# Kernel optimization log

Measured on AMD Instinct MI355X. Metric: run time of the kernel, lower is better.

The kernel has to match this reference:

```python
import jax, jax.numpy as jnp
import numpy as np
import math

TOPK = 32

def setup_inputs() -> dict:
    key = jax.random.key(0)
    k1, k2, k3, k4 = jax.random.split(key, 4)
    B, D_e, D_o, T, H, W = 2, 128, 256, 16, 64, 64
    H_ref = W_ref = 32  # resolution_ref = 2
    THW_ref = T * H_ref * W_ref
    HW_ref = H_ref * W_ref
    return {
        "m_in": jax.random.normal(k1, (B, D_e, T, H, W), jnp.float32),
        "m_out": jax.random.normal(k2, (B, D_o, T, H, W), jnp.float32),
        "q_in": jax.random.normal(k3, (B, D_e, H, W), jnp.float32),
        "qk_ref": jax.random.normal(k4, (B, THW_ref, HW_ref), jnp.float32),
    }


def reference(m_in, m_out, q_in, qk_ref):
    B, D_e, T, H, W = m_in.shape
    D_o = m_out.shape[1]
    _, THW_ref, HW_ref = qk_ref.shape
    res = int(math.sqrt(H * W // HW_ref))
    H_ref, W_ref = H // res, W // res
    s = res
    k = TOPK

    # top-k memory blocks for each of the HW_ref query blocks
    topk_val, topk_idx = jax.lax.top_k(jnp.swapaxes(qk_ref, 1, 2), k)  # [B, HW_ref, k]
    # torch path scatters one-hot then uses nonzero -> gather order is ascending-index;
    # softmax-attention over n is permutation invariant, but sort for exact faithfulness.
    idx_sorted = jnp.sort(topk_idx, axis=-1)

    def blockify(m, D):
        # [B,D,T,H,W] -> [B, T*H_ref*W_ref, s, s, D]
        m = m.reshape(B, D, T, H_ref, s, W_ref, s)
        m = m.transpose(0, 2, 3, 5, 4, 6, 1)  # B,T,H_ref,W_ref,s,s,D
        return m.reshape(B, T * H_ref * W_ref, s, s, D)

    m_in_b = blockify(m_in, D_e)
    m_out_b = blockify(m_out, D_o)

    flat_idx = idx_sorted.reshape(B, HW_ref * k)
    gather = jax.vmap(lambda mb, i: mb[i])  # per-batch fancy gather of blocks
    m_in_sel = gather(m_in_b, flat_idx).reshape(B, H_ref, W_ref, k * s * s, D_e)
    m_out_sel = gather(m_out_b, flat_idx).reshape(B, H_ref, W_ref, k * s * s, D_o)

    # query blocks: [B, H_ref, W_ref, D_e, s, s]
    q = q_in.reshape(B, D_e, H_ref, s, W_ref, s).transpose(0, 2, 4, 1, 3, 5)

    p = jnp.einsum('bhwnc,bhwcij->bhwijn', m_in_sel, q) / math.sqrt(D_e)
    p = jax.nn.softmax(p, axis=-1)
    mem_out = jnp.einsum('bhwnc,bhwijn->bchiwj', m_out_sel, p).reshape(B, D_o, H, W)

    kk = max(k // 4, 1)
    return mem_out, topk_idx[:, :, :kk], topk_val[:, :, :kk]
```

## Files before the change

kernel.cpp:

```cpp
#include <hip/hip_runtime.h>
#include <math.h>



__global__ __launch_bounds__(256) void transpose_qk(const float* __restrict__ in,
                                                    float* __restrict__ out) {
    __shared__ float tile[64][65];
    int r0 = blockIdx.x * 64;
    int q0 = blockIdx.y * 64;
    int b  = blockIdx.z;
    const float* src = in  + (size_t)b * 16384 * 1024;
    float*       dst = out + (size_t)b * 1024 * 16384;
    int tx = threadIdx.x & 63;
    int ty = threadIdx.x >> 6;
#pragma unroll
    for (int i = 0; i < 16; ++i) {
        int r = ty + i * 4;
        tile[r][tx] = src[(size_t)(r0 + r) * 1024 + q0 + tx];
    }
    __syncthreads();
#pragma unroll
    for (int i = 0; i < 16; ++i) {
        int q = ty + i * 4;
        dst[(size_t)(q0 + q) * 16384 + r0 + tx] = tile[tx][q];
    }
}

__device__ inline unsigned mono_u32(float f) {
    unsigned b = __float_as_uint(f);
    return (b & 0x80000000u) ? ~b : (b | 0x80000000u);
}

__global__ __launch_bounds__(512) void topk_kernel(const float* __restrict__ qk_T,
                                                   float* __restrict__ out_idx,
                                                   float* __restrict__ out_val,
                                                   int* __restrict__ idx_sorted) {
    int bid = blockIdx.x;
    int tid = threadIdx.x;
    const float4* row4 = (const float4*)(qk_T + (size_t)bid * 16384);

    float v[32];
#pragma unroll
    for (int g = 0; g < 8; ++g) {
        float4 t4 = row4[g * 512 + tid];
        v[g * 4 + 0] = t4.x; v[g * 4 + 1] = t4.y;
        v[g * 4 + 2] = t4.z; v[g * 4 + 3] = t4.w;
    }

    float cv = v[0]; int ci = 0;
#pragma unroll
    for (int e = 1; e < 32; ++e) { if (v[e] > cv) { cv = v[e]; ci = e; } }

    __shared__ int hist1[256];
    __shared__ int hist2[256];
    __shared__ int s_b1, s_above1, s_cnt;
    __shared__ unsigned s_tu;
    __shared__ unsigned long long cand[512];
    __shared__ unsigned long long selk[32];
    __shared__ float wvf[2][8];
    __shared__ int   wif[2][8];

    if (tid < 256) { hist1[tid] = 0; hist2[tid] = 0; }
    if (tid == 0) s_cnt = 0;
    __syncthreads();

    unsigned um = mono_u32(cv);
    atomicAdd(&hist1[um >> 24], 1);
    __syncthreads();

    if (tid < 64) {
        int base = 252 - 4 * tid;
        int h0 = hist1[base], h1 = hist1[base + 1], h2 = hist1[base + 2], h3 = hist1[base + 3];
        int gs = h0 + h1 + h2 + h3;
        int pre = gs;
#pragma unroll
        for (int off = 1; off < 64; off <<= 1) {
            int o = __shfl_up(pre, off, 64);
            if (tid >= off) pre += o;
        }
        int excl = pre - gs;
        if (excl < 32 && pre >= 32) {
            int c = excl, b, ab;
            c += h3; if (c >= 32) { b = base + 3; ab = c - h3; }
            else { c += h2; if (c >= 32) { b = base + 2; ab = c - h2; }
            else { c += h1; if (c >= 32) { b = base + 1; ab = c - h1; }
            else { c += h0;   b = base;     ab = c - h0; } } }
            s_b1 = b; s_above1 = ab;
        }
    }
    __syncthreads();
    int b1 = s_b1;
    if ((int)(um >> 24) == b1) atomicAdd(&hist2[(um >> 16) & 0xFF], 1);
    __syncthreads();

    if (tid < 64) {
        int A = s_above1;
        int base = 252 - 4 * tid;
        int h0 = hist2[base], h1 = hist2[base + 1], h2 = hist2[base + 2], h3 = hist2[base + 3];
        int gs = h0 + h1 + h2 + h3;
        int pre = gs;
#pragma unroll
        for (int off = 1; off < 64; off <<= 1) {
            int o = __shfl_up(pre, off, 64);
            if (tid >= off) pre += o;
        }
        int excl = pre - gs;
        if (A + excl < 32 && A + pre >= 32) {
            int c = A + excl, b;
            c += h3; if (c >= 32) b = base + 3;
            else { c += h2; if (c >= 32) b = base + 2;
            else { c += h1; if (c >= 32) b = base + 1;
            else { b = base; } } }
            s_tu = (((unsigned)b1 << 8) | (unsigned)b) << 16;
        }
    }
    __syncthreads();
    unsigned tu = s_tu;

#pragma unroll
    for (int e = 0; e < 32; ++e) {
        unsigned ue = mono_u32(v[e]);
        if (ue >= tu) {
            int pos = atomicAdd(&s_cnt, 1);
            if (pos < 512) {
                int gi = (e >> 2) * 2048 + tid * 4 + (e & 3);
                cand[pos] = ((unsigned long long)ue << 32) |
                            (unsigned long long)(16383 - gi);
            }
        }
    }
    __syncthreads();
    int C = s_cnt;

    if (C <= 512) {
        if (tid < C) {
            unsigned long long mine = cand[tid];
            int rank = 0;
            for (int j = 0; j < C; ++j) rank += (cand[j] > mine) ? 1 : 0;
            if (rank < 32) selk[rank] = mine;
        }
        __syncthreads();
    } else {
        unsigned used = 0u;
        int w = tid >> 6, lane = tid & 63;
#pragma unroll 1
        for (int s = 0; s < 32; ++s) {
            float rv = cv; int ri = (ci >> 2) * 2048 + tid * 4 + (ci & 3);
#pragma unroll
            for (int off = 32; off >= 1; off >>= 1) {
                float ov = __shfl_xor(rv, off, 64);
                int   oi = __shfl_xor(ri, off, 64);
                if (ov > rv || (ov == rv && oi < ri)) { rv = ov; ri = oi; }
            }
            int buf = s & 1;
            if (lane == 0) { wvf[buf][w] = rv; wif[buf][w] = ri; }
            __syncthreads();
            float bv = wvf[buf][0]; int bi = wif[buf][0];
#pragma unroll
            for (int j = 1; j < 8; ++j) {
                float jv = wvf[buf][j]; int ji = wif[buf][j];
                if (jv > bv || (jv == bv && ji < bi)) { bv = jv; bi = ji; }
            }
            if (tid == 0)
                selk[s] = ((unsigned long long)mono_u32(bv) << 32) |
                          (unsigned long long)(16383 - bi);
            if (((bi >> 2) & 511) == tid) {
                int be = ((bi >> 11) << 2) | (bi & 3);
                used |= 1u << be;
                cv = -__builtin_inff(); ci = 0;
#pragma unroll
                for (int e = 0; e < 32; ++e)
                    if (!((used >> e) & 1u) && v[e] > cv) { cv = v[e]; ci = e; }
            }
        }
        __syncthreads();
    }

    if (tid < 8) {
        unsigned long long k = selk[tid];
        unsigned uv = (unsigned)(k >> 32);
        unsigned bits = (uv & 0x80000000u) ? (uv ^ 0x80000000u) : ~uv;
        out_val[(size_t)bid * 8 + tid] = __uint_as_float(bits);
        int gi = 16383 - (int)(k & 0xFFFFFFFFull);
        out_idx[(size_t)bid * 8 + tid] = (float)gi;
    }
    if (tid < 32) {
        int mine = 16383 - (int)(selk[tid] & 0xFFFFFFFFull);
        int rank = 0;
#pragma unroll
        for (int j = 0; j < 32; ++j) {
            int oj = 16383 - (int)(selk[j] & 0xFFFFFFFFull);
            rank += (oj < mine) ? 1 : 0;
        }
        idx_sorted[(size_t)bid * 32 + rank] = mine;
    }
}

template <int D, int T>
__global__ __launch_bounds__(256) void blockify_tiled(const float* __restrict__ in,
                                                      float* __restrict__ out) {
    constexpr int NCH = D / 64;
    int wg = blockIdx.x;
    int ch = wg % NCH;
    int hb = (wg / NCH) % 32;
    int t  = (wg / (NCH * 32)) % T;
    int b  = wg / (NCH * 32 * T);
    int c0 = ch * 64;
    int tid = threadIdx.x;

    __shared__ float tile[64][129];

    {
        int x = tid & 63;
        int rw = tid >> 6;
#pragma unroll 8
        for (int i = 0; i < 32; ++i) {
            int r = i * 4 + rw;
            int c = r >> 1, si = r & 1;
            tile[c][si * 64 + x] =
                in[((((size_t)b * D + c0 + c) * T + t) * 64 + (2 * hb + si)) * 64 + x];
        }
    }
    __syncthreads();

    {
        int p = tid >> 6;
        int cc = tid & 63;
        int si = p >> 1, sj = p & 1;
        size_t nbase = (((size_t)b * T + t) * 1024 + (size_t)hb * 32);
#pragma unroll 8
        for (int wb = 0; wb < 32; ++wb) {
            out[(nbase + wb) * 4 * D + (size_t)p * D + c0 + cc] =
                tile[cc][si * 64 + 2 * wb + sj];
        }
    }
}

__global__ __launch_bounds__(256) void attn_kernel(const float* __restrict__ m_in_b,
                                                   const float* __restrict__ m_out_b,
                                                   const float* __restrict__ q_b,
                                                   const int* __restrict__ idx_sorted,
                                                   float* __restrict__ out) {
    int bid = blockIdx.x;
    int b = bid >> 10, qblk = bid & 1023;
    int hb = qblk >> 5, wb = qblk & 31;
    int tid = threadIdx.x;
    int w = tid >> 6, lane = tid & 63;

    __shared__ float K[64][129];
    __shared__ float Q[4][128];
    __shared__ float P[4][128];
    __shared__ int   blks[32];

    if (tid < 32) blks[tid] = idx_sorted[(size_t)bid * 32 + tid];
    {
        const float* qsrc = q_b + (size_t)bid * 512;
        ((float*)Q)[tid]       = qsrc[tid];
        ((float*)Q)[tid + 256] = qsrc[tid + 256];
    }
    __syncthreads();

    const float scale = 0.08838834764831845f;
    float s01[2];
#pragma unroll 1
    for (int half = 0; half < 2; ++half) {
        if (half) __syncthreads();
#pragma unroll 4
        for (int ki = 0; ki < 16; ++ki) {
            int blk = blks[half * 16 + ki];
            const float* src = m_in_b + ((size_t)b * 16384 + blk) * 512;
            int p0 = tid >> 7, c0 = tid & 127;
            K[ki * 4 + p0][c0]     = src[tid];
            K[ki * 4 + p0 + 2][c0] = src[tid + 256];
        }
        __syncthreads();
        float acc = 0.f;
#pragma unroll 4
        for (int c = 0; c < 128; ++c) acc += K[lane][c] * Q[w][c];
        s01[half] = acc * scale;
    }

    float m = fmaxf(s01[0], s01[1]);
#pragma unroll
    for (int off = 32; off >= 1; off >>= 1) m = fmaxf(m, __shfl_xor(m, off, 64));
    float e0 = expf(s01[0] - m), e1 = expf(s01[1] - m);
    float sum = e0 + e1;
#pragma unroll
    for (int off = 32; off >= 1; off >>= 1) sum += __shfl_xor(sum, off, 64);
    float inv = 1.0f / sum;
    P[w][lane]      = e0 * inv;
    P[w][lane + 64] = e1 * inv;
    __syncthreads();

    float a0 = 0.f, a1 = 0.f, a2 = 0.f, a3 = 0.f;
    int d = tid;
#pragma unroll 1
    for (int ki = 0; ki < 32; ++ki) {
        const float* vsrc = m_out_b + ((size_t)b * 16384 + blks[ki]) * 1024;
#pragma unroll
        for (int p = 0; p < 4; ++p) {
            float vv = vsrc[p * 256 + d];
            int n = ki * 4 + p;
            a0 += P[0][n] * vv; a1 += P[1][n] * vv;
            a2 += P[2][n] * vv; a3 += P[3][n] * vv;
        }
    }
    size_t base = (((size_t)b * 256 + d) * 64 + hb * 2) * 64 + wb * 2;
    out[base]      = a0;
    out[base + 1]  = a1;
    out[base + 64] = a2;
    out[base + 65] = a3;
}

extern "C" void kernel_launch(void* const* d_in, const int* in_sizes, int n_in,
                              void* d_out, int out_size, void* d_ws, size_t ws_size,
                              hipStream_t stream) {
    const float* m_in  = (const float*)d_in[0];
    const float* m_out = (const float*)d_in[1];
    const float* q_in  = (const float*)d_in[2];
    const float* qk    = (const float*)d_in[3];

    char* ws = (char*)d_ws;
    float* qk_T    = (float*)(ws);
    float* m_out_b = (float*)(ws);
    float* m_in_b  = (float*)(ws + 134217728);
    float* q_b     = (float*)(ws + 201326592);
    int*   idxs    = (int*)  (ws + 205520896);

    float* out     = (float*)d_out;
    float* out_mem = out;
    float* out_idx = out + 2097152;
    float* out_val = out + 2113536;

    transpose_qk<<<dim3(256, 16, 2), 256, 0, stream>>>(qk, qk_T);
    topk_kernel<<<2048, 512, 0, stream>>>(qk_T, out_idx, out_val, idxs);
    blockify_tiled<128, 16><<<2 * 16 * 32 * 2, 256, 0, stream>>>(m_in, m_in_b);
    blockify_tiled<128, 1><<<2 * 1 * 32 * 2, 256, 0, stream>>>(q_in, q_b);
    blockify_tiled<256, 16><<<2 * 16 * 32 * 4, 256, 0, stream>>>(m_out, m_out_b);
    attn_kernel<<<2048, 256, 0, stream>>>(m_in_b, m_out_b, q_b, idxs, out_mem);
}
```

Measured before the change: 466.9 us.

## Replace qk transpose plus radix top-k with chunk-max threshold filter

Removes the full transpose of qk_ref. Top-k now works directly on the column layout: per-chunk maxima, then a threshold taken as the 32nd-largest chunk max, then a global atomic candidate filter, then a small per-column selection. This removes one full write and one full read of the 128MB score matrix. In exchange it adds several launches, global atomics, and a slow fallback that rescans the whole column when candidates overflow.

```diff
diff --git a/kernel.cpp b/kernel.cpp
--- a/kernel.cpp
+++ b/kernel.cpp
@@ -2,178 +2,131 @@
 #include <math.h>
 
 
-
-__global__ __launch_bounds__(256) void transpose_qk(const float* __restrict__ in,
-                                                    float* __restrict__ out) {
-    __shared__ float tile[64][65];
-    int r0 = blockIdx.x * 64;
-    int q0 = blockIdx.y * 64;
-    int b  = blockIdx.z;
-    const float* src = in  + (size_t)b * 16384 * 1024;
-    float*       dst = out + (size_t)b * 1024 * 16384;
-    int tx = threadIdx.x & 63;
-    int ty = threadIdx.x >> 6;
-#pragma unroll
-    for (int i = 0; i < 16; ++i) {
-        int r = ty + i * 4;
-        tile[r][tx] = src[(size_t)(r0 + r) * 1024 + q0 + tx];
-    }
-    __syncthreads();
-#pragma unroll
-    for (int i = 0; i < 16; ++i) {
-        int q = ty + i * 4;
-        dst[(size_t)(q0 + q) * 16384 + r0 + tx] = tile[tx][q];
-    }
-}
 
 __device__ inline unsigned mono_u32(float f) {
     unsigned b = __float_as_uint(f);
     return (b & 0x80000000u) ? ~b : (b | 0x80000000u);
 }
 
-__global__ __launch_bounds__(512) void topk_kernel(const float* __restrict__ qk_T,
+__global__ __launch_bounds__(256) void qk_chunk_max(const float* __restrict__ qk,
+                                                    float* __restrict__ Mx) {
+    int wg = blockIdx.x;
+    int cg = wg & 3;
+    int chunk = (wg >> 2) & 63;
+    int b = wg >> 8;
+    int col = cg * 256 + threadIdx.x;
+    const float* p = qk + ((size_t)b * 16384 + (size_t)chunk * 256) * 1024 + col;
+    float m = -__builtin_inff();
+#pragma unroll
+    for (int rb = 0; rb < 16; ++rb) {
+        float vv[16];
+#pragma unroll
+        for (int u = 0; u < 16; ++u)
+            vv[u] = p[(size_t)(rb * 16 + u) * 1024];
+#pragma unroll
+        for (int u = 0; u < 16; ++u) m = fmaxf(m, vv[u]);
+    }
+    Mx[((size_t)b * 1024 + col) * 64 + chunk] = m;
+}
+
+__global__ __launch_bounds__(256) void qk_thresh(const float* __restrict__ Mx,
+                                                 unsigned* __restrict__ t_u,
+                                                 int* __restrict__ cnt) {
+    int g = blockIdx.x * 256 + threadIdx.x;
+    if (g < 2048) cnt[g] = 0;
+    int colg = blockIdx.x * 4 + (threadIdx.x >> 6);
+    int lane = threadIdx.x & 63;
+    float mv = Mx[(size_t)colg * 64 + lane];
+    unsigned long long key = ((unsigned long long)mono_u32(mv) << 32) | (unsigned)lane;
+    int rank = 0;
+#pragma unroll 8
+    for (int j = 0; j < 64; ++j) {
+        unsigned long long other = __shfl(key, j, 64);
+        rank += (other > key) ? 1 : 0;
+    }
+    if (rank == 31) t_u[colg] = (unsigned)(key >> 32);
+}
+
+__global__ __launch_bounds__(256) void qk_filter(const float* __restrict__ qk,
+                                                 const unsigned* __restrict__ t_u,
+                                                 int* __restrict__ cnt,
+                                                 unsigned long long* __restrict__ cand) {
+    int wg = blockIdx.x;
+    int cg = wg & 3;
+    int chunk = (wg >> 2) & 63;
+    int b = wg >> 8;
+    int col = cg * 256 + threadIdx.x;
+    int colg = b * 1024 + col;
+    unsigned t = t_u[colg];
+    const float* p = qk + ((size_t)b * 16384 + (size_t)chunk * 256) * 1024 + col;
+    int n0 = chunk * 256;
+#pragma unroll
+    for (int rb = 0; rb < 16; ++rb) {
+        float vv[16];
+#pragma unroll
+        for (int u = 0; u < 16; ++u)
+            vv[u] = p[(size_t)(rb * 16 + u) * 1024];
+#pragma unroll
+        for (int u = 0; u < 16; ++u) {
+            unsigned uu = mono_u32(vv[u]);
+            if (uu >= t) {
+                int pos = atomicAdd(&cnt[colg], 1);
+                if (pos < 256) {
+                    int gi = n0 + rb * 16 + u;
+                    cand[(size_t)colg * 256 + pos] =
+                        ((unsigned long long)uu << 32) |
+                        (unsigned long long)(16383 - gi);
+                }
+            }
+        }
+    }
+}
+
+__global__ __launch_bounds__(256) void topk_select(const unsigned long long* __restrict__ cand,
+                                                   const int* __restrict__ cnt,
+                                                   const float* __restrict__ qk,
                                                    float* __restrict__ out_idx,
                                                    float* __restrict__ out_val,
                                                    int* __restrict__ idx_sorted) {
     int bid = blockIdx.x;
     int tid = threadIdx.x;
-    const float4* row4 = (const float4*)(qk_T + (size_t)bid * 16384);
-
-    float v[32];
-#pragma unroll
-    for (int g = 0; g < 8; ++g) {
-        float4 t4 = row4[g * 512 + tid];
-        v[g * 4 + 0] = t4.x; v[g * 4 + 1] = t4.y;
-        v[g * 4 + 2] = t4.z; v[g * 4 + 3] = t4.w;
-    }
-
-    float cv = v[0]; int ci = 0;
-#pragma unroll
-    for (int e = 1; e < 32; ++e) { if (v[e] > cv) { cv = v[e]; ci = e; } }
-
-    __shared__ int hist1[256];
-    __shared__ int hist2[256];
-    __shared__ int s_b1, s_above1, s_cnt;
-    __shared__ unsigned s_tu;
-    __shared__ unsigned long long cand[512];
+    __shared__ unsigned long long sc[256];
     __shared__ unsigned long long selk[32];
-    __shared__ float wvf[2][8];
-    __shared__ int   wif[2][8];
-
-    if (tid < 256) { hist1[tid] = 0; hist2[tid] = 0; }
-    if (tid == 0) s_cnt = 0;
-    __syncthreads();
-
-    unsigned um = mono_u32(cv);
-    atomicAdd(&hist1[um >> 24], 1);
-    __syncthreads();
-
-    if (tid < 64) {
-        int base = 252 - 4 * tid;
-        int h0 = hist1[base], h1 = hist1[base + 1], h2 = hist1[base + 2], h3 = hist1[base + 3];
-        int gs = h0 + h1 + h2 + h3;
-        int pre = gs;
-#pragma unroll
-        for (int off = 1; off < 64; off <<= 1) {
-            int o = __shfl_up(pre, off, 64);
-            if (tid >= off) pre += o;
-        }
-        int excl = pre - gs;
-        if (excl < 32 && pre >= 32) {
-            int c = excl, b, ab;
-            c += h3; if (c >= 32) { b = base + 3; ab = c - h3; }
-            else { c += h2; if (c >= 32) { b = base + 2; ab = c - h2; }
-            else { c += h1; if (c >= 32) { b = base + 1; ab = c - h1; }
-            else { c += h0;   b = base;     ab = c - h0; } } }
-            s_b1 = b; s_above1 = ab;
-        }
-    }
-    __syncthreads();
-    int b1 = s_b1;
-    if ((int)(um >> 24) == b1) atomicAdd(&hist2[(um >> 16) & 0xFF], 1);
-    __syncthreads();
-
-    if (tid < 64) {
-        int A = s_above1;
-        int base = 252 - 4 * tid;
-        int h0 = hist2[base], h1 = hist2[base + 1], h2 = hist2[base + 2], h3 = hist2[base + 3];
-        int gs = h0 + h1 + h2 + h3;
-        int pre = gs;
-#pragma unroll
-        for (int off = 1; off < 64; off <<= 1) {
-            int o = __shfl_up(pre, off, 64);
-            if (tid >= off) pre += o;
-        }
-        int excl = pre - gs;
-        if (A + excl < 32 && A + pre >= 32) {
-            int c = A + excl, b;
-            c += h3; if (c >= 32) b = base + 3;
-            else { c += h2; if (c >= 32) b = base + 2;
-            else { c += h1; if (c >= 32) b = base + 1;
-            else { b = base; } } }
-            s_tu = (((unsigned)b1 << 8) | (unsigned)b) << 16;
-        }
-    }
-    __syncthreads();
-    unsigned tu = s_tu;
-
-#pragma unroll
-    for (int e = 0; e < 32; ++e) {
-        unsigned ue = mono_u32(v[e]);
-        if (ue >= tu) {
-            int pos = atomicAdd(&s_cnt, 1);
-            if (pos < 512) {
-                int gi = (e >> 2) * 2048 + tid * 4 + (e & 3);
-                cand[pos] = ((unsigned long long)ue << 32) |
-                            (unsigned long long)(16383 - gi);
-            }
-        }
-    }
-    __syncthreads();
-    int C = s_cnt;
-
-    if (C <= 512) {
+
+    int C = cnt[bid];
+    if (C <= 256) {
+        if (tid < C) sc[tid] = cand[(size_t)bid * 256 + tid];
+        __syncthreads();
         if (tid < C) {
-            unsigned long long mine = cand[tid];
+            unsigned long long mine = sc[tid];
             int rank = 0;
-            for (int j = 0; j < C; ++j) rank += (cand[j] > mine) ? 1 : 0;
+            for (int j = 0; j < C; ++j) rank += (sc[j] > mine) ? 1 : 0;
             if (rank < 32) selk[rank] = mine;
         }
         __syncthreads();
     } else {
-        unsigned used = 0u;
-        int w = tid >> 6, lane = tid & 63;
+        int b = bid >> 10, q = bid & 1023;
+        const float* colp = qk + (size_t)b * 16384 * 1024 + q;
+        unsigned long long prev = ~0ull;
 #pragma unroll 1
         for (int s = 0; s < 32; ++s) {
-            float rv = cv; int ri = (ci >> 2) * 2048 + tid * 4 + (ci & 3);
-#pragma unroll
-            for (int off = 32; off >= 1; off >>= 1) {
-                float ov = __shfl_xor(rv, off, 64);
-                int   oi = __shfl_xor(ri, off, 64);
-                if (ov > rv || (ov == rv && oi < ri)) { rv = ov; ri = oi; }
+            unsigned long long best = 0;
+            for (int r = tid; r < 16384; r += 256) {
+                unsigned long long k =
+                    ((unsigned long long)mono_u32(colp[(size_t)r * 1024]) << 32) |
+                    (unsigned long long)(16383 - r);
+                if (k < prev && k > best) best = k;
             }
-            int buf = s & 1;
-            if (lane == 0) { wvf[buf][w] = rv; wif[buf][w] = ri; }
+            sc[tid] = best;
             __syncthreads();
-            float bv = wvf[buf][0]; int bi = wif[buf][0];
-#pragma unroll
-            for (int j = 1; j < 8; ++j) {
-                float jv = wvf[buf][j]; int ji = wif[buf][j];
-                if (jv > bv || (jv == bv && ji < bi)) { bv = jv; bi = ji; }
+            for (int off = 128; off >= 1; off >>= 1) {
+                if (tid < off && sc[tid + off] > sc[tid]) sc[tid] = sc[tid + off];
+                __syncthreads();
             }
-            if (tid == 0)
-                selk[s] = ((unsigned long long)mono_u32(bv) << 32) |
-                          (unsigned long long)(16383 - bi);
-            if (((bi >> 2) & 511) == tid) {
-                int be = ((bi >> 11) << 2) | (bi & 3);
-                used |= 1u << be;
-                cv = -__builtin_inff(); ci = 0;
-#pragma unroll
-                for (int e = 0; e < 32; ++e)
-                    if (!((used >> e) & 1u) && v[e] > cv) { cv = v[e]; ci = e; }
-            }
-        }
-        __syncthreads();
+            if (tid == 0) selk[s] = sc[0];
+            __syncthreads();
+            prev = selk[s];
+        }
     }
 
     if (tid < 8) {
@@ -321,19 +274,26 @@
     const float* qk    = (const float*)d_in[3];
 
     char* ws = (char*)d_ws;
-    float* qk_T    = (float*)(ws);
     float* m_out_b = (float*)(ws);
     float* m_in_b  = (float*)(ws + 134217728);
     float* q_b     = (float*)(ws + 201326592);
     int*   idxs    = (int*)  (ws + 205520896);
 
+    unsigned long long* cand = (unsigned long long*)(ws);
+    float*    Mx  = (float*)   (ws + 4194304);
+    unsigned* t_u = (unsigned*)(ws + 4718592);
+    int*      cnt = (int*)     (ws + 4726784);
+
     float* out     = (float*)d_out;
     float* out_mem = out;
     float* out_idx = out + 2097152;
     float* out_val = out + 2113536;
 
-    transpose_qk<<<dim3(256, 16, 2), 256, 0, stream>>>(qk, qk_T);
-    topk_kernel<<<2048, 512, 0, stream>>>(qk_T, out_idx, out_val, idxs);
+    qk_chunk_max<<<512, 256, 0, stream>>>(qk, Mx);
+    qk_thresh   <<<512, 256, 0, stream>>>(Mx, t_u, cnt);
+    qk_filter   <<<512, 256, 0, stream>>>(qk, t_u, cnt, cand);
+    topk_select <<<2048, 256, 0, stream>>>(cand, cnt, qk, out_idx, out_val, idxs);
+
     blockify_tiled<128, 16><<<2 * 16 * 32 * 2, 256, 0, stream>>>(m_in, m_in_b);
     blockify_tiled<128, 1><<<2 * 1 * 32 * 2, 256, 0, stream>>>(q_in, q_b);
     blockify_tiled<256, 16><<<2 * 16 * 32 * 4, 256, 0, stream>>>(m_out, m_out_b);
```

New measurement: 473.2 us. Within noise of the previous version (+1.4%).
